# Kernel tuning notes

Measured on AMD Instinct MI355X. Metric: run time of the kernel, lower is better.

## Reference

```python
import jax, jax.numpy as jnp
import numpy as np

B, N, E, D, H, O = 4, 10000, 160000, 128, 4, 64
NEG_SLOPE = 0.2  # PyG GATConv default


def setup_inputs() -> dict:
    key = jax.random.key(0)
    ks = jax.random.split(key, 9)
    x = jax.random.normal(ks[0], (B, N, D), jnp.float32)
    edge_index = jax.random.randint(ks[1], (2, E), 0, N, dtype=jnp.int64)
    edge_attr = jax.random.uniform(ks[2], (E,), jnp.float32)
    W_src = jax.random.normal(ks[3], (D, H, O), jnp.float32) * (1.0 / np.sqrt(D))
    att_src = jax.random.normal(ks[4], (H, O), jnp.float32) * 0.1
    att_dst = jax.random.normal(ks[5], (H, O), jnp.float32) * 0.1
    W_edge = jax.random.normal(ks[6], (H, O), jnp.float32) * 0.1  # lin_edge weight for edge_dim=1
    att_edge = jax.random.normal(ks[7], (H, O), jnp.float32) * 0.1
    bias = jnp.zeros((O,), jnp.float32)
    return {"x": x, "edge_index": edge_index, "edge_attr": edge_attr,
            "W_src": W_src, "att_src": att_src, "att_dst": att_dst,
            "W_edge": W_edge, "att_edge": att_edge, "bias": bias}


def reference(x, edge_index, edge_attr, W_src, att_src, att_dst, W_edge, att_edge, bias):
    src, dst = edge_index[0], edge_index[1]
    # shared linear projection (PyG non-bipartite GATConv): [B,N,H,O]
    h = jnp.einsum('bnd,dho->bnho', x, W_src)
    a_src = jnp.einsum('bnho,ho->bnh', h, att_src)  # [B,N,H]
    a_dst = jnp.einsum('bnho,ho->bnh', h, att_dst)  # [B,N,H]
    # edge feature projection (edge_dim=1): [E,H]
    a_edge = edge_attr[:, None] * jnp.einsum('ho,ho->h', W_edge, att_edge)[None, :]
    # attention logits per edge: [B,E,H]
    alpha = a_src[:, src] + a_dst[:, dst] + a_edge[None]
    alpha = jax.nn.leaky_relu(alpha, NEG_SLOPE)
    # segment softmax over destination nodes; segment ops need axis 0 = E
    alpha_t = jnp.transpose(alpha, (1, 0, 2))  # [E,B,H]
    m = jax.ops.segment_max(alpha_t, dst, num_segments=N)  # [N,B,H]
    m = jnp.where(jnp.isfinite(m), m, 0.0)
    p = jnp.exp(alpha_t - m[dst])
    s = jax.ops.segment_sum(p, dst, num_segments=N)
    w = p / jnp.maximum(s[dst], jnp.asarray(1e-16, p.dtype))  # [E,B,H]
    # weighted messages from source nodes, scatter-add into destinations
    msg = w[..., None] * jnp.transpose(h[:, src], (1, 0, 2, 3))  # [E,B,H,O]
    out = jax.ops.segment_sum(msg, dst, num_segments=N)  # [N,B,H,O]
    out = out.mean(axis=2) + bias  # concat=False -> mean over heads, [N,B,O]
    return jnp.transpose(out, (1, 0, 2))  # [B,N,O]
```

## Files before the change

### kernel.cpp

```cpp
#include <hip/hip_runtime.h>
#include <hip/hip_bf16.h>
#include <math.h>

constexpr int B_  = 4;
constexpr int N_  = 10000;
constexpr int E_  = 160000;
constexpr int D_  = 128;
constexpr int H_  = 4;
constexpr int O_  = 64;
constexpr float NEG_SLOPE = 0.2f;

using short8 = __attribute__((ext_vector_type(8))) short;
using f32x4  = __attribute__((ext_vector_type(4))) float;

static __device__ __forceinline__ unsigned short f2bf(float f) {
    unsigned u = __float_as_uint(f);
    u += 0x7fffu + ((u >> 16) & 1u);
    return (unsigned short)(u >> 16);
}
static __device__ __forceinline__ float bf2f(unsigned short h) {
    return __uint_as_float((unsigned)h << 16);
}

__global__ __launch_bounds__(256) void k_prep(
    const float* __restrict__ Wsrc, const float* __restrict__ att_src,
    const float* __restrict__ att_dst,
    const float* __restrict__ W_edge, const float* __restrict__ att_edge,
    unsigned short* __restrict__ W1t,
    float* __restrict__ vsrc, float* __restrict__ vdst,
    int* __restrict__ deg, float* __restrict__ c)
{
    const int d = blockIdx.x;
    const int t = threadIdx.x;
    const int h = t >> 6;

    for (int i = d * 256 + t; i < N_; i += 128 * 256) deg[i] = 0;

    const float wv = Wsrc[(size_t)d * 256 + t];
    const int cc = ((t & 63) << 2) | h;
    W1t[(size_t)cc * 128 + d] = f2bf(wv);

    float vs = wv * att_src[t];
    float vd = wv * att_dst[t];
#pragma unroll
    for (int off = 32; off > 0; off >>= 1) {
        vs += __shfl_down(vs, off, 64);
        vd += __shfl_down(vd, off, 64);
    }
    if ((t & 63) == 0) {
        vsrc[d * 4 + h] = vs;
        vdst[d * 4 + h] = vd;
    }

    if (d == 0) {
        float v = W_edge[t] * att_edge[t];
#pragma unroll
        for (int off = 32; off > 0; off >>= 1) v += __shfl_down(v, off, 64);
        if ((t & 63) == 0) c[h] = v;
    }
}

__global__ __launch_bounds__(256) void k_gemm(
    const float* __restrict__ x, const int* __restrict__ ei,
    const unsigned short* __restrict__ W1t,
    const float* __restrict__ vsrc, const float* __restrict__ vdst,
    unsigned short* __restrict__ hbw, float* __restrict__ asrc, float* __restrict__ adst,
    int* __restrict__ deg, int* __restrict__ rank)
{
    constexpr int ROWS = 32;
    constexpr int APAD = 136;
    __shared__ uint4 SHq[1024];
    __shared__ float4 vsL[128];
    __shared__ float4 vdL[128];
    unsigned short* A1 = (unsigned short*)SHq;
    unsigned short* Cb = (unsigned short*)SHq;

    const int t = threadIdx.x;
    const int w = t >> 6;
    const int lane = t & 63;
    const int i = lane & 15;
    const int q = lane >> 4;
    const size_t rowbase = (size_t)blockIdx.x * ROWS;

    short8 breg[4][4];
#pragma unroll
    for (int ks = 0; ks < 4; ++ks)
#pragma unroll
        for (int ctl = 0; ctl < 4; ++ctl) {
            const size_t boff = (size_t)((w * 4 + ctl) * 16 + i) * 128 + ks * 32 + q * 8;
            breg[ks][ctl] = *(const short8*)&W1t[boff];
        }

    {
        const float4* xg = (const float4*)(x + rowbase * D_);
#pragma unroll
        for (int it = 0; it < 4; ++it) {
            const int idx = it * 256 + t;
            const int row = idx >> 5;
            const int c4  = idx & 31;
            float4 xv = xg[idx];
            ushort4 h1;
            h1.x = f2bf(xv.x); h1.y = f2bf(xv.y);
            h1.z = f2bf(xv.z); h1.w = f2bf(xv.w);
            *(ushort4*)&A1[row * APAD + c4 * 4] = h1;
        }
        if (t < 128) vsL[t] = ((const float4*)vsrc)[t];
        else         vdL[t - 128] = ((const float4*)vdst)[t - 128];
    }
    __syncthreads();

    f32x4 acc[2][4];
#pragma unroll
    for (int tl = 0; tl < 2; ++tl)
#pragma unroll
        for (int ctl = 0; ctl < 4; ++ctl) acc[tl][ctl] = (f32x4){0.f, 0.f, 0.f, 0.f};

#pragma unroll
    for (int ks = 0; ks < 4; ++ks) {
        const int a0off = i * APAD + ks * 32 + q * 8;
        const int a1off = (16 + i) * APAD + ks * 32 + q * 8;
        short8 at0 = *(const short8*)&A1[a0off];
        short8 at1 = *(const short8*)&A1[a1off];
#pragma unroll
        for (int ctl = 0; ctl < 4; ++ctl) {
            acc[0][ctl] = __builtin_amdgcn_mfma_f32_16x16x32_bf16(at0, breg[ks][ctl], acc[0][ctl], 0, 0, 0);
            acc[1][ctl] = __builtin_amdgcn_mfma_f32_16x16x32_bf16(at1, breg[ks][ctl], acc[1][ctl], 0, 0, 0);
        }
    }

    {
        const int r = lane >> 3, g = lane & 7;
        const int row_l = w * 8 + r;
        float s0 = 0, s1 = 0, s2 = 0, s3 = 0, d0 = 0, d1 = 0, d2 = 0, d3 = 0;
#pragma unroll
        for (int dd4 = 0; dd4 < 4; ++dd4) {
            const int db = g * 16 + dd4 * 4;
            ushort4 u1 = *(const ushort4*)&A1[row_l * APAD + db];
            const float xv0 = bf2f(u1.x);
            const float xv1 = bf2f(u1.y);
            const float xv2 = bf2f(u1.z);
            const float xv3 = bf2f(u1.w);
            float4 vsa = vsL[db + 0], vda = vdL[db + 0];
            float4 vsb = vsL[db + 1], vdb = vdL[db + 1];
            float4 vsc = vsL[db + 2], vdc = vdL[db + 2];
            float4 vsd = vsL[db + 3], vdd = vdL[db + 3];
            s0 = fmaf(xv0, vsa.x, s0); s1 = fmaf(xv0, vsa.y, s1);
            s2 = fmaf(xv0, vsa.z, s2); s3 = fmaf(xv0, vsa.w, s3);
            d0 = fmaf(xv0, vda.x, d0); d1 = fmaf(xv0, vda.y, d1);
            d2 = fmaf(xv0, vda.z, d2); d3 = fmaf(xv0, vda.w, d3);
            s0 = fmaf(xv1, vsb.x, s0); s1 = fmaf(xv1, vsb.y, s1);
            s2 = fmaf(xv1, vsb.z, s2); s3 = fmaf(xv1, vsb.w, s3);
            d0 = fmaf(xv1, vdb.x, d0); d1 = fmaf(xv1, vdb.y, d1);
            d2 = fmaf(xv1, vdb.z, d2); d3 = fmaf(xv1, vdb.w, d3);
            s0 = fmaf(xv2, vsc.x, s0); s1 = fmaf(xv2, vsc.y, s1);
            s2 = fmaf(xv2, vsc.z, s2); s3 = fmaf(xv2, vsc.w, s3);
            d0 = fmaf(xv2, vdc.x, d0); d1 = fmaf(xv2, vdc.y, d1);
            d2 = fmaf(xv2, vdc.z, d2); d3 = fmaf(xv2, vdc.w, d3);
            s0 = fmaf(xv3, vsd.x, s0); s1 = fmaf(xv3, vsd.y, s1);
            s2 = fmaf(xv3, vsd.z, s2); s3 = fmaf(xv3, vsd.w, s3);
            d0 = fmaf(xv3, vdd.x, d0); d1 = fmaf(xv3, vdd.y, d1);
            d2 = fmaf(xv3, vdd.z, d2); d3 = fmaf(xv3, vdd.w, d3);
        }
#pragma unroll
        for (int off = 4; off > 0; off >>= 1) {
            s0 += __shfl_down(s0, off, 64); s1 += __shfl_down(s1, off, 64);
            s2 += __shfl_down(s2, off, 64); s3 += __shfl_down(s3, off, 64);
            d0 += __shfl_down(d0, off, 64); d1 += __shfl_down(d1, off, 64);
            d2 += __shfl_down(d2, off, 64); d3 += __shfl_down(d3, off, 64);
        }
        if (g == 0) {
            const size_t rg = rowbase + row_l;
            *(float4*)&asrc[rg * 4] = make_float4(s0, s1, s2, s3);
            *(float4*)&adst[rg * 4] = make_float4(d0, d1, d2, d3);
        }
    }

    __syncthreads();
#pragma unroll
    for (int tl = 0; tl < 2; ++tl) {
#pragma unroll
        for (int ctl = 0; ctl < 4; ++ctl) {
            const int col = (w * 4 + ctl) * 16 + i;
            const int chnk = col >> 3;
            const int within = col & 7;
#pragma unroll
            for (int r = 0; r < 4; ++r) {
                const int row = tl * 16 + q * 4 + r;
                const int s = chnk ^ row;
                Cb[row * 256 + s * 8 + within] = f2bf(acc[tl][ctl][r]);
            }
        }
    }
    __syncthreads();
    {
        const int chnk = t & 31;
#pragma unroll
        for (int k = 0; k < 4; ++k) {
            const int row = k * 8 + (t >> 5);
            const int s = chnk ^ row;
            const uint4 v = *(const uint4*)&Cb[row * 256 + s * 8];
            *(uint4*)&hbw[(rowbase + row) * 256 + chnk * 8] = v;
        }
    }

    if (t < 128) {
        const int ee = blockIdx.x * 128 + t;
        rank[ee] = atomicAdd(&deg[ei[E_ + ee]], 1);
    }
}

__global__ __launch_bounds__(1024) void k_scan(const int* __restrict__ deg,
                                               int* __restrict__ rowptr)
{
    __shared__ int wsum[16], wexcl[16];
    const int t = threadIdx.x, wv = t >> 6, ln = t & 63;
    const int base = t * 10;
    int v[10];
    int tot = 0;
    if (base < N_) {
#pragma unroll
        for (int i = 0; i < 10; ++i) { v[i] = deg[base + i]; tot += v[i]; }
    }
    int incl = tot;
#pragma unroll
    for (int off = 1; off < 64; off <<= 1) {
        int u = __shfl_up(incl, off, 64);
        if (ln >= off) incl += u;
    }
    if (ln == 63) wsum[wv] = incl;
    __syncthreads();
    if (wv == 0 && ln < 16) {
        int s = wsum[ln];
        int si = s;
#pragma unroll
        for (int off = 1; off < 16; off <<= 1) {
            int u = __shfl_up(si, off, 64);
            if (ln >= off) si += u;
        }
        wexcl[ln] = si - s;
    }
    __syncthreads();
    if (base < N_) {
        int run = wexcl[wv] + incl - tot;
#pragma unroll
        for (int i = 0; i < 10; ++i) {
            rowptr[base + i] = run; run += v[i];
        }
    }
    if (t == 0) rowptr[N_] = E_;
}

__global__ __launch_bounds__(256) void k_place(
    const int* __restrict__ ei, const float* __restrict__ eattr,
    const int* __restrict__ rowptr, const int* __restrict__ rank,
    int2* __restrict__ srcea)
{
    const int e = blockIdx.x * 256 + threadIdx.x;
    if (e >= E_) return;
    const int dst = ei[E_ + e];
    const int pos = rowptr[dst] + rank[e];
    srcea[pos] = make_int2(ei[e], __float_as_int(eattr[e]));
}

__global__ __launch_bounds__(256) void k_agg(
    const int* __restrict__ rowptr, const int2* __restrict__ srcea,
    const float* __restrict__ asrc, const float* __restrict__ adst,
    const float* __restrict__ cvec, const unsigned short* __restrict__ hbu,
    const float* __restrict__ bias, float* __restrict__ out)
{
    __shared__ float pS[4][64][4];
    __shared__ int   baseS[4][64];

    const int b    = blockIdx.x & 3;
    const int g    = blockIdx.x >> 2;
    const int wave = threadIdx.x >> 6;
    const int lane = threadIdx.x & 63;
    const int dst  = g * 4 + wave;

    const int start = rowptr[dst];
    const int end   = rowptr[dst + 1];

    const float4 ad = *(const float4*)&adst[((size_t)b * N_ + dst) * 4];
    const float4 cc = *(const float4*)cvec;

    float a0[4] = {0.f, 0.f, 0.f, 0.f};
    float a1[4] = {0.f, 0.f, 0.f, 0.f};
    float a2[4] = {0.f, 0.f, 0.f, 0.f};
    float a3[4] = {0.f, 0.f, 0.f, 0.f};
    float q0 = 0.f, q1 = 0.f, q2 = 0.f, q3 = 0.f;

    for (int c0 = start; c0 < end; c0 += 64) {
        const int jl = c0 + lane;
        const bool valid = jl < end;
        const int2 rec = srcea[valid ? jl : start];
        const int   srcl = rec.x;
        const float ea   = __int_as_float(rec.y);
        const float4 as = *(const float4*)&asrc[((size_t)b * N_ + srcl) * 4];
        float4 al;
        al.x = as.x + ad.x + ea * cc.x;
        al.y = as.y + ad.y + ea * cc.y;
        al.z = as.z + ad.z + ea * cc.z;
        al.w = as.w + ad.w + ea * cc.w;
        al.x = al.x > 0.f ? al.x : NEG_SLOPE * al.x;
        al.y = al.y > 0.f ? al.y : NEG_SLOPE * al.y;
        al.z = al.z > 0.f ? al.z : NEG_SLOPE * al.z;
        al.w = al.w > 0.f ? al.w : NEG_SLOPE * al.w;
        const float px = valid ? __expf(al.x) : 0.f;
        const float py = valid ? __expf(al.y) : 0.f;
        const float pz = valid ? __expf(al.z) : 0.f;
        const float pw = valid ? __expf(al.w) : 0.f;
        q0 += px; q1 += py; q2 += pz; q3 += pw;

        *(float4*)&pS[wave][lane][0] = make_float4(px, py, pz, pw);
        baseS[wave][lane] = (b * N_ + srcl) << 8;
        __builtin_amdgcn_wave_barrier();

        const int cnt = min(64, end - c0);
        const int lo4 = lane * 4;
        int j = 0;
        for (; j + 4 <= cnt; j += 4) {
            const float4 p0 = *(const float4*)&pS[wave][j + 0][0];
            const float4 p1 = *(const float4*)&pS[wave][j + 1][0];
            const float4 p2 = *(const float4*)&pS[wave][j + 2][0];
            const float4 p3 = *(const float4*)&pS[wave][j + 3][0];
            const int r0 = baseS[wave][j + 0];
            const int r1 = baseS[wave][j + 1];
            const int r2 = baseS[wave][j + 2];
            const int r3 = baseS[wave][j + 3];
            const ushort4 h0 = *(const ushort4*)&hbu[(size_t)r0 + lo4];
            const ushort4 h1 = *(const ushort4*)&hbu[(size_t)r1 + lo4];
            const ushort4 h2 = *(const ushort4*)&hbu[(size_t)r2 + lo4];
            const ushort4 h3 = *(const ushort4*)&hbu[(size_t)r3 + lo4];
            a0[0] = fmaf(p0.x, bf2f(h0.x), a0[0]);
            a0[1] = fmaf(p0.y, bf2f(h0.y), a0[1]);
            a0[2] = fmaf(p0.z, bf2f(h0.z), a0[2]);
            a0[3] = fmaf(p0.w, bf2f(h0.w), a0[3]);
            a1[0] = fmaf(p1.x, bf2f(h1.x), a1[0]);
            a1[1] = fmaf(p1.y, bf2f(h1.y), a1[1]);
            a1[2] = fmaf(p1.z, bf2f(h1.z), a1[2]);
            a1[3] = fmaf(p1.w, bf2f(h1.w), a1[3]);
            a2[0] = fmaf(p2.x, bf2f(h2.x), a2[0]);
            a2[1] = fmaf(p2.y, bf2f(h2.y), a2[1]);
            a2[2] = fmaf(p2.z, bf2f(h2.z), a2[2]);
            a2[3] = fmaf(p2.w, bf2f(h2.w), a2[3]);
            a3[0] = fmaf(p3.x, bf2f(h3.x), a3[0]);
            a3[1] = fmaf(p3.y, bf2f(h3.y), a3[1]);
            a3[2] = fmaf(p3.z, bf2f(h3.z), a3[2]);
            a3[3] = fmaf(p3.w, bf2f(h3.w), a3[3]);
        }
        for (; j < cnt; ++j) {
            const float4 p0 = *(const float4*)&pS[wave][j][0];
            const int    r0 = baseS[wave][j];
            const ushort4 h0 = *(const ushort4*)&hbu[(size_t)r0 + lo4];
            a0[0] = fmaf(p0.x, bf2f(h0.x), a0[0]);
            a0[1] = fmaf(p0.y, bf2f(h0.y), a0[1]);
            a0[2] = fmaf(p0.z, bf2f(h0.z), a0[2]);
            a0[3] = fmaf(p0.w, bf2f(h0.w), a0[3]);
        }
        __builtin_amdgcn_wave_barrier();
    }

#pragma unroll
    for (int off = 32; off > 0; off >>= 1) {
        q0 += __shfl_xor(q0, off, 64);
        q1 += __shfl_xor(q1, off, 64);
        q2 += __shfl_xor(q2, off, 64);
        q3 += __shfl_xor(q3, off, 64);
    }

    const float r = (a0[0] + a1[0] + a2[0] + a3[0]) / fmaxf(q0, 1e-16f)
                  + (a0[1] + a1[1] + a2[1] + a3[1]) / fmaxf(q1, 1e-16f)
                  + (a0[2] + a1[2] + a2[2] + a3[2]) / fmaxf(q2, 1e-16f)
                  + (a0[3] + a1[3] + a2[3] + a3[3]) / fmaxf(q3, 1e-16f);
    out[((size_t)b * N_ + dst) * O_ + lane] = 0.25f * r + bias[lane];
}

extern "C" void kernel_launch(void* const* d_in, const int* in_sizes, int n_in,
                              void* d_out, int out_size, void* d_ws, size_t ws_size,
                              hipStream_t stream)
{
    (void)in_sizes; (void)n_in; (void)out_size; (void)ws_size;
    const float* x        = (const float*)d_in[0];
    const int*   ei       = (const int*)d_in[1];
    const float* eattr    = (const float*)d_in[2];
    const float* Wsrc     = (const float*)d_in[3];
    const float* att_src  = (const float*)d_in[4];
    const float* att_dst  = (const float*)d_in[5];
    const float* W_edge   = (const float*)d_in[6];
    const float* att_edge = (const float*)d_in[7];
    const float* bias     = (const float*)d_in[8];
    float* out = (float*)d_out;

    char* w = (char*)d_ws;
    auto take = [&](size_t bytes) { char* p = w; w += (bytes + 15) & ~size_t(15); return p; };
    unsigned short* hb   = (unsigned short*)take((size_t)B_ * N_ * O_ * H_ * 2);
    float* asrc    = (float*)take((size_t)B_ * N_ * H_ * 4);
    float* adst    = (float*)take((size_t)B_ * N_ * H_ * 4);
    float* c       = (float*)take(4 * 4);
    unsigned short* W1t = (unsigned short*)take((size_t)256 * 128 * 2);
    float* vsrc    = (float*)take((size_t)128 * 4 * 4);
    float* vdst    = (float*)take((size_t)128 * 4 * 4);
    int* deg       = (int*)take((size_t)N_ * 4);
    int* rowptr    = (int*)take((size_t)(N_ + 1) * 4);
    int* rank      = (int*)take((size_t)E_ * 4);
    int2* srcea    = (int2*)take((size_t)E_ * 8);

    hipLaunchKernelGGL(k_prep, dim3(128), dim3(256), 0, stream,
                       Wsrc, att_src, att_dst, W_edge, att_edge,
                       W1t, vsrc, vdst, deg, c);
    hipLaunchKernelGGL(k_gemm, dim3((B_ * N_) / 32), dim3(256), 0, stream,
                       x, ei, W1t, vsrc, vdst, hb, asrc, adst, deg, rank);
    hipLaunchKernelGGL(k_scan, dim3(1), dim3(1024), 0, stream, deg, rowptr);
    hipLaunchKernelGGL(k_place, dim3((E_ + 255) / 256), dim3(256), 0, stream,
                       ei, eattr, rowptr, rank, srcea);
    hipLaunchKernelGGL(k_agg, dim3(N_ / 4 * B_), dim3(256), 0, stream,
                       rowptr, srcea, asrc, adst, c, hb, bias, out);
}
```

Baseline: 162.0 us.

## Switch to fp16, compute attention scores via MFMA, fuse scan into placement

Switches the projected features and weights from bf16 to fp16. The per-node attention scores are now computed with an extra MFMA against a packed fp16 attention-vector matrix, replacing the scalar FMA reduction in LDS. It also merges the single-block scan and the edge placement into one kernel: block 0 computes rowptr and the other blocks spin on a release/acquire flag. This removes one launch and the scalar dot-product work, at the cost of fp16 range and precision risk and a spin-wait that relies on block 0 being scheduled.

```diff
diff --git a/kernel.cpp b/kernel.cpp
--- a/kernel.cpp
+++ b/kernel.cpp
@@ -1,5 +1,5 @@
 #include <hip/hip_runtime.h>
-#include <hip/hip_bf16.h>
+#include <hip/hip_fp16.h>
 #include <math.h>
 
 constexpr int B_  = 4;
@@ -10,25 +10,22 @@
 constexpr int O_  = 64;
 constexpr float NEG_SLOPE = 0.2f;
 
-using short8 = __attribute__((ext_vector_type(8))) short;
-using f32x4  = __attribute__((ext_vector_type(4))) float;
-
-static __device__ __forceinline__ unsigned short f2bf(float f) {
-    unsigned u = __float_as_uint(f);
-    u += 0x7fffu + ((u >> 16) & 1u);
-    return (unsigned short)(u >> 16);
-}
-static __device__ __forceinline__ float bf2f(unsigned short h) {
-    return __uint_as_float((unsigned)h << 16);
+using half8 = __attribute__((ext_vector_type(8))) _Float16;
+using f32x4 = __attribute__((ext_vector_type(4))) float;
+
+static __device__ __forceinline__ unsigned short f2h(float f) {
+    return __half_as_ushort(__float2half(f));
+}
+static __device__ __forceinline__ float h2f(unsigned short u) {
+    return __half2float(__ushort_as_half(u));
 }
 
 __global__ __launch_bounds__(256) void k_prep(
     const float* __restrict__ Wsrc, const float* __restrict__ att_src,
     const float* __restrict__ att_dst,
     const float* __restrict__ W_edge, const float* __restrict__ att_edge,
-    unsigned short* __restrict__ W1t,
-    float* __restrict__ vsrc, float* __restrict__ vdst,
-    int* __restrict__ deg, float* __restrict__ c)
+    unsigned short* __restrict__ W1t, unsigned short* __restrict__ Vt,
+    int* __restrict__ deg, float* __restrict__ c, int* __restrict__ flag)
 {
     const int d = blockIdx.x;
     const int t = threadIdx.x;
@@ -38,7 +35,7 @@
 
     const float wv = Wsrc[(size_t)d * 256 + t];
     const int cc = ((t & 63) << 2) | h;
-    W1t[(size_t)cc * 128 + d] = f2bf(wv);
+    W1t[(size_t)cc * 128 + d] = f2h(wv);
 
     float vs = wv * att_src[t];
     float vd = wv * att_dst[t];
@@ -48,11 +45,16 @@
         vd += __shfl_down(vd, off, 64);
     }
     if ((t & 63) == 0) {
-        vsrc[d * 4 + h] = vs;
-        vdst[d * 4 + h] = vd;
+        Vt[h * 128 + d]       = f2h(vs);
+        Vt[(4 + h) * 128 + d] = f2h(vd);
+    }
+    if (d == 1) {
+#pragma unroll
+        for (int k = 0; k < 4; ++k) Vt[1024 + k * 256 + t] = 0;
     }
 
     if (d == 0) {
+        if (t == 0) flag[0] = 0;
         float v = W_edge[t] * att_edge[t];
 #pragma unroll
         for (int off = 32; off > 0; off >>= 1) v += __shfl_down(v, off, 64);
@@ -62,16 +64,13 @@
 
 __global__ __launch_bounds__(256) void k_gemm(
     const float* __restrict__ x, const int* __restrict__ ei,
-    const unsigned short* __restrict__ W1t,
-    const float* __restrict__ vsrc, const float* __restrict__ vdst,
+    const unsigned short* __restrict__ W1t, const unsigned short* __restrict__ Vt,
     unsigned short* __restrict__ hbw, float* __restrict__ asrc, float* __restrict__ adst,
     int* __restrict__ deg, int* __restrict__ rank)
 {
     constexpr int ROWS = 32;
     constexpr int APAD = 136;
     __shared__ uint4 SHq[1024];
-    __shared__ float4 vsL[128];
-    __shared__ float4 vdL[128];
     unsigned short* A1 = (unsigned short*)SHq;
     unsigned short* Cb = (unsigned short*)SHq;
 
@@ -82,14 +81,20 @@
     const int q = lane >> 4;
     const size_t rowbase = (size_t)blockIdx.x * ROWS;
 
-    short8 breg[4][4];
+    half8 breg[4][4];
 #pragma unroll
     for (int ks = 0; ks < 4; ++ks)
 #pragma unroll
         for (int ctl = 0; ctl < 4; ++ctl) {
             const size_t boff = (size_t)((w * 4 + ctl) * 16 + i) * 128 + ks * 32 + q * 8;
-            breg[ks][ctl] = *(const short8*)&W1t[boff];
-        }
+            breg[ks][ctl] = *(const half8*)&W1t[boff];
+        }
+    half8 vreg[4];
+    if (w < 2) {
+#pragma unroll
+        for (int ks = 0; ks < 4; ++ks)
+            vreg[ks] = *(const half8*)&Vt[i * 128 + ks * 32 + q * 8];
+    }
 
     {
         const float4* xg = (const float4*)(x + rowbase * D_);
@@ -100,12 +105,10 @@
             const int c4  = idx & 31;
             float4 xv = xg[idx];
             ushort4 h1;
-            h1.x = f2bf(xv.x); h1.y = f2bf(xv.y);
-            h1.z = f2bf(xv.z); h1.w = f2bf(xv.w);
+            h1.x = f2h(xv.x); h1.y = f2h(xv.y);
+            h1.z = f2h(xv.z); h1.w = f2h(xv.w);
             *(ushort4*)&A1[row * APAD + c4 * 4] = h1;
         }
-        if (t < 128) vsL[t] = ((const float4*)vsrc)[t];
-        else         vdL[t - 128] = ((const float4*)vdst)[t - 128];
     }
     __syncthreads();
 
@@ -114,64 +117,32 @@
     for (int tl = 0; tl < 2; ++tl)
 #pragma unroll
         for (int ctl = 0; ctl < 4; ++ctl) acc[tl][ctl] = (f32x4){0.f, 0.f, 0.f, 0.f};
+    f32x4 accV = (f32x4){0.f, 0.f, 0.f, 0.f};
 
 #pragma unroll
     for (int ks = 0; ks < 4; ++ks) {
         const int a0off = i * APAD + ks * 32 + q * 8;
         const int a1off = (16 + i) * APAD + ks * 32 + q * 8;
-        short8 at0 = *(const short8*)&A1[a0off];
-        short8 at1 = *(const short8*)&A1[a1off];
+        half8 at0 = *(const half8*)&A1[a0off];
+        half8 at1 = *(const half8*)&A1[a1off];
 #pragma unroll
         for (int ctl = 0; ctl < 4; ++ctl) {
-            acc[0][ctl] = __builtin_amdgcn_mfma_f32_16x16x32_bf16(at0, breg[ks][ctl], acc[0][ctl], 0, 0, 0);
-            acc[1][ctl] = __builtin_amdgcn_mfma_f32_16x16x32_bf16(at1, breg[ks][ctl], acc[1][ctl], 0, 0, 0);
-        }
-    }
-
-    {
-        const int r = lane >> 3, g = lane & 7;
-        const int row_l = w * 8 + r;
-        float s0 = 0, s1 = 0, s2 = 0, s3 = 0, d0 = 0, d1 = 0, d2 = 0, d3 = 0;
-#pragma unroll
-        for (int dd4 = 0; dd4 < 4; ++dd4) {
-            const int db = g * 16 + dd4 * 4;
-            ushort4 u1 = *(const ushort4*)&A1[row_l * APAD + db];
-            const float xv0 = bf2f(u1.x);
-            const float xv1 = bf2f(u1.y);
-            const float xv2 = bf2f(u1.z);
-            const float xv3 = bf2f(u1.w);
-            float4 vsa = vsL[db + 0], vda = vdL[db + 0];
-            float4 vsb = vsL[db + 1], vdb = vdL[db + 1];
-            float4 vsc = vsL[db + 2], vdc = vdL[db + 2];
-            float4 vsd = vsL[db + 3], vdd = vdL[db + 3];
-            s0 = fmaf(xv0, vsa.x, s0); s1 = fmaf(xv0, vsa.y, s1);
-            s2 = fmaf(xv0, vsa.z, s2); s3 = fmaf(xv0, vsa.w, s3);
-            d0 = fmaf(xv0, vda.x, d0); d1 = fmaf(xv0, vda.y, d1);
-            d2 = fmaf(xv0, vda.z, d2); d3 = fmaf(xv0, vda.w, d3);
-            s0 = fmaf(xv1, vsb.x, s0); s1 = fmaf(xv1, vsb.y, s1);
-            s2 = fmaf(xv1, vsb.z, s2); s3 = fmaf(xv1, vsb.w, s3);
-            d0 = fmaf(xv1, vdb.x, d0); d1 = fmaf(xv1, vdb.y, d1);
-            d2 = fmaf(xv1, vdb.z, d2); d3 = fmaf(xv1, vdb.w, d3);
-            s0 = fmaf(xv2, vsc.x, s0); s1 = fmaf(xv2, vsc.y, s1);
-            s2 = fmaf(xv2, vsc.z, s2); s3 = fmaf(xv2, vsc.w, s3);
-            d0 = fmaf(xv2, vdc.x, d0); d1 = fmaf(xv2, vdc.y, d1);
-            d2 = fmaf(xv2, vdc.z, d2); d3 = fmaf(xv2, vdc.w, d3);
-            s0 = fmaf(xv3, vsd.x, s0); s1 = fmaf(xv3, vsd.y, s1);
-            s2 = fmaf(xv3, vsd.z, s2); s3 = fmaf(xv3, vsd.w, s3);
-            d0 = fmaf(xv3, vdd.x, d0); d1 = fmaf(xv3, vdd.y, d1);
-            d2 = fmaf(xv3, vdd.z, d2); d3 = fmaf(xv3, vdd.w, d3);
-        }
-#pragma unroll
-        for (int off = 4; off > 0; off >>= 1) {
-            s0 += __shfl_down(s0, off, 64); s1 += __shfl_down(s1, off, 64);
-            s2 += __shfl_down(s2, off, 64); s3 += __shfl_down(s3, off, 64);
-            d0 += __shfl_down(d0, off, 64); d1 += __shfl_down(d1, off, 64);
-            d2 += __shfl_down(d2, off, 64); d3 += __shfl_down(d3, off, 64);
-        }
-        if (g == 0) {
-            const size_t rg = rowbase + row_l;
-            *(float4*)&asrc[rg * 4] = make_float4(s0, s1, s2, s3);
-            *(float4*)&adst[rg * 4] = make_float4(d0, d1, d2, d3);
+            acc[0][ctl] = __builtin_amdgcn_mfma_f32_16x16x32_f16(at0, breg[ks][ctl], acc[0][ctl], 0, 0, 0);
+            acc[1][ctl] = __builtin_amdgcn_mfma_f32_16x16x32_f16(at1, breg[ks][ctl], acc[1][ctl], 0, 0, 0);
+        }
+        if (w < 2) {
+            const half8 atV = (w == 0) ? at0 : at1;
+            accV = __builtin_amdgcn_mfma_f32_16x16x32_f16(atV, vreg[ks], accV, 0, 0, 0);
+        }
+    }
+
+    if (w < 2 && i < 8) {
+#pragma unroll
+        for (int r = 0; r < 4; ++r) {
+            const int row = w * 16 + q * 4 + r;
+            const size_t rg = rowbase + row;
+            if (i < 4) asrc[rg * 4 + i]       = accV[r];
+            else       adst[rg * 4 + (i - 4)] = accV[r];
         }
     }
 
@@ -187,7 +158,7 @@
             for (int r = 0; r < 4; ++r) {
                 const int row = tl * 16 + q * 4 + r;
                 const int s = chnk ^ row;
-                Cb[row * 256 + s * 8 + within] = f2bf(acc[tl][ctl][r]);
+                Cb[row * 256 + s * 8 + within] = f2h(acc[tl][ctl][r]);
             }
         }
     }
@@ -209,57 +180,78 @@
     }
 }
 
-__global__ __launch_bounds__(1024) void k_scan(const int* __restrict__ deg,
-                                               int* __restrict__ rowptr)
-{
-    __shared__ int wsum[16], wexcl[16];
-    const int t = threadIdx.x, wv = t >> 6, ln = t & 63;
-    const int base = t * 10;
-    int v[10];
-    int tot = 0;
-    if (base < N_) {
-#pragma unroll
-        for (int i = 0; i < 10; ++i) { v[i] = deg[base + i]; tot += v[i]; }
-    }
-    int incl = tot;
-#pragma unroll
-    for (int off = 1; off < 64; off <<= 1) {
-        int u = __shfl_up(incl, off, 64);
-        if (ln >= off) incl += u;
-    }
-    if (ln == 63) wsum[wv] = incl;
-    __syncthreads();
-    if (wv == 0 && ln < 16) {
-        int s = wsum[ln];
-        int si = s;
-#pragma unroll
-        for (int off = 1; off < 16; off <<= 1) {
-            int u = __shfl_up(si, off, 64);
-            if (ln >= off) si += u;
-        }
-        wexcl[ln] = si - s;
-    }
-    __syncthreads();
-    if (base < N_) {
-        int run = wexcl[wv] + incl - tot;
-#pragma unroll
-        for (int i = 0; i < 10; ++i) {
-            rowptr[base + i] = run; run += v[i];
-        }
-    }
-    if (t == 0) rowptr[N_] = E_;
-}
-
-__global__ __launch_bounds__(256) void k_place(
+__global__ __launch_bounds__(256) void k_scanplace(
     const int* __restrict__ ei, const float* __restrict__ eattr,
-    const int* __restrict__ rowptr, const int* __restrict__ rank,
+    const int* __restrict__ deg, const int* __restrict__ rank,
+    int* __restrict__ rowptr, int* __restrict__ flag,
     int2* __restrict__ srcea)
 {
-    const int e = blockIdx.x * 256 + threadIdx.x;
-    if (e >= E_) return;
-    const int dst = ei[E_ + e];
-    const int pos = rowptr[dst] + rank[e];
-    srcea[pos] = make_int2(ei[e], __float_as_int(eattr[e]));
+    const int t = threadIdx.x;
+    const int e = blockIdx.x * 256 + t;
+
+    int src = 0, dst = 0, rk = 0; float ea = 0.f;
+    if (e < E_) {
+        src = ei[e]; dst = ei[E_ + e]; rk = rank[e]; ea = eattr[e];
+    }
+
+    if (blockIdx.x == 0) {
+        __shared__ int wsum[4], wexcl[4];
+        const int wv = t >> 6, ln = t & 63;
+        const int b4 = t * 10;
+        const int4* dg4 = (const int4*)deg;
+        int4 v[10];
+        int tot = 0;
+#pragma unroll
+        for (int k = 0; k < 10; ++k) {
+            if (b4 + k < 2500) {
+                v[k] = dg4[b4 + k];
+                tot += v[k].x + v[k].y + v[k].z + v[k].w;
+            } else v[k] = make_int4(0, 0, 0, 0);
+        }
+        int incl = tot;
+#pragma unroll
+        for (int off = 1; off < 64; off <<= 1) {
+            int u = __shfl_up(incl, off, 64);
+            if (ln >= off) incl += u;
+        }
+        if (ln == 63) wsum[wv] = incl;
+        __syncthreads();
+        if (t < 4) {
+            int s = 0;
+            for (int k = 0; k < t; ++k) s += wsum[k];
+            wexcl[t] = s;
+        }
+        __syncthreads();
+        int run = wexcl[wv] + incl - tot;
+#pragma unroll
+        for (int k = 0; k < 10; ++k) {
+            if (b4 + k < 2500) {
+                int4 w4;
+                w4.x = run; run += v[k].x;
+                w4.y = run; run += v[k].y;
+                w4.z = run; run += v[k].z;
+                w4.w = run; run += v[k].w;
+                *(int4*)&rowptr[(b4 + k) * 4] = w4;
+            }
+        }
+        if (t == 0) rowptr[N_] = E_;
+        __threadfence();
+        __syncthreads();
+        if (t == 0)
+            __hip_atomic_store(flag, 1, __ATOMIC_RELEASE, __HIP_MEMORY_SCOPE_AGENT);
+    } else {
+        if (t == 0) {
+            while (__hip_atomic_load(flag, __ATOMIC_ACQUIRE, __HIP_MEMORY_SCOPE_AGENT) == 0)
+                __builtin_amdgcn_s_sleep(2);
+        }
+        __syncthreads();
+    }
+
+    if (e < E_) {
+        const int rp = __hip_atomic_load(&rowptr[dst], __ATOMIC_RELAXED,
+                                         __HIP_MEMORY_SCOPE_AGENT);
+        srcea[rp + rk] = make_int2(src, __float_as_int(ea));
+    }
 }
 
 __global__ __launch_bounds__(256) void k_agg(
@@ -331,31 +323,31 @@
             const ushort4 h1 = *(const ushort4*)&hbu[(size_t)r1 + lo4];
             const ushort4 h2 = *(const ushort4*)&hbu[(size_t)r2 + lo4];
             const ushort4 h3 = *(const ushort4*)&hbu[(size_t)r3 + lo4];
-            a0[0] = fmaf(p0.x, bf2f(h0.x), a0[0]);
-            a0[1] = fmaf(p0.y, bf2f(h0.y), a0[1]);
-            a0[2] = fmaf(p0.z, bf2f(h0.z), a0[2]);
-            a0[3] = fmaf(p0.w, bf2f(h0.w), a0[3]);
-            a1[0] = fmaf(p1.x, bf2f(h1.x), a1[0]);
-            a1[1] = fmaf(p1.y, bf2f(h1.y), a1[1]);
-            a1[2] = fmaf(p1.z, bf2f(h1.z), a1[2]);
-            a1[3] = fmaf(p1.w, bf2f(h1.w), a1[3]);
-            a2[0] = fmaf(p2.x, bf2f(h2.x), a2[0]);
-            a2[1] = fmaf(p2.y, bf2f(h2.y), a2[1]);
-            a2[2] = fmaf(p2.z, bf2f(h2.z), a2[2]);
-            a2[3] = fmaf(p2.w, bf2f(h2.w), a2[3]);
-            a3[0] = fmaf(p3.x, bf2f(h3.x), a3[0]);
-            a3[1] = fmaf(p3.y, bf2f(h3.y), a3[1]);
-            a3[2] = fmaf(p3.z, bf2f(h3.z), a3[2]);
-            a3[3] = fmaf(p3.w, bf2f(h3.w), a3[3]);
+            a0[0] = fmaf(p0.x, h2f(h0.x), a0[0]);
+            a0[1] = fmaf(p0.y, h2f(h0.y), a0[1]);
+            a0[2] = fmaf(p0.z, h2f(h0.z), a0[2]);
+            a0[3] = fmaf(p0.w, h2f(h0.w), a0[3]);
+            a1[0] = fmaf(p1.x, h2f(h1.x), a1[0]);
+            a1[1] = fmaf(p1.y, h2f(h1.y), a1[1]);
+            a1[2] = fmaf(p1.z, h2f(h1.z), a1[2]);
+            a1[3] = fmaf(p1.w, h2f(h1.w), a1[3]);
+            a2[0] = fmaf(p2.x, h2f(h2.x), a2[0]);
+            a2[1] = fmaf(p2.y, h2f(h2.y), a2[1]);
+            a2[2] = fmaf(p2.z, h2f(h2.z), a2[2]);
+            a2[3] = fmaf(p2.w, h2f(h2.w), a2[3]);
+            a3[0] = fmaf(p3.x, h2f(h3.x), a3[0]);
+            a3[1] = fmaf(p3.y, h2f(h3.y), a3[1]);
+            a3[2] = fmaf(p3.z, h2f(h3.z), a3[2]);
+            a3[3] = fmaf(p3.w, h2f(h3.w), a3[3]);
         }
         for (; j < cnt; ++j) {
             const float4 p0 = *(const float4*)&pS[wave][j][0];
             const int    r0 = baseS[wave][j];
             const ushort4 h0 = *(const ushort4*)&hbu[(size_t)r0 + lo4];
-            a0[0] = fmaf(p0.x, bf2f(h0.x), a0[0]);
-            a0[1] = fmaf(p0.y, bf2f(h0.y), a0[1]);
-            a0[2] = fmaf(p0.z, bf2f(h0.z), a0[2]);
-            a0[3] = fmaf(p0.w, bf2f(h0.w), a0[3]);
+            a0[0] = fmaf(p0.x, h2f(h0.x), a0[0]);
+            a0[1] = fmaf(p0.y, h2f(h0.y), a0[1]);
+            a0[2] = fmaf(p0.z, h2f(h0.z), a0[2]);
+            a0[3] = fmaf(p0.w, h2f(h0.w), a0[3]);
         }
         __builtin_amdgcn_wave_barrier();
     }
@@ -398,21 +390,20 @@
     float* adst    = (float*)take((size_t)B_ * N_ * H_ * 4);
     float* c       = (float*)take(4 * 4);
     unsigned short* W1t = (unsigned short*)take((size_t)256 * 128 * 2);
-    float* vsrc    = (float*)take((size_t)128 * 4 * 4);
-    float* vdst    = (float*)take((size_t)128 * 4 * 4);
+    unsigned short* Vt  = (unsigned short*)take((size_t)16 * 128 * 2);
     int* deg       = (int*)take((size_t)N_ * 4);
     int* rowptr    = (int*)take((size_t)(N_ + 1) * 4);
     int* rank      = (int*)take((size_t)E_ * 4);
+    int* flag      = (int*)take(16);
     int2* srcea    = (int2*)take((size_t)E_ * 8);
 
     hipLaunchKernelGGL(k_prep, dim3(128), dim3(256), 0, stream,
                        Wsrc, att_src, att_dst, W_edge, att_edge,
-                       W1t, vsrc, vdst, deg, c);
+                       W1t, Vt, deg, c, flag);
     hipLaunchKernelGGL(k_gemm, dim3((B_ * N_) / 32), dim3(256), 0, stream,
-                       x, ei, W1t, vsrc, vdst, hb, asrc, adst, deg, rank);
-    hipLaunchKernelGGL(k_scan, dim3(1), dim3(1024), 0, stream, deg, rowptr);
-    hipLaunchKernelGGL(k_place, dim3((E_ + 255) / 256), dim3(256), 0, stream,
-                       ei, eattr, rowptr, rank, srcea);
+                       x, ei, W1t, Vt, hb, asrc, adst, deg, rank);
+    hipLaunchKernelGGL(k_scanplace, dim3((E_ + 255) / 256), dim3(256), 0, stream,
+                       ei, eattr, deg, rank, rowptr, flag, srcea);
     hipLaunchKernelGGL(k_agg, dim3(N_ / 4 * B_), dim3(256), 0, stream,
                        rowptr, srcea, asrc, adst, c, hb, bias, out);
 }
```

New measurement: 248.7 us. 1.53x slower.
